# Performance work log

Hardware: AMD Instinct MI355X
Metric: run time of the kernel (lower is better)

## Reference

```python
import jax, jax.numpy as jnp
import numpy as np

B, T, C = 64, 256, 384
H = 6
D = C // H  # head_size = 64


def setup_inputs() -> dict:
    key = jax.random.key(0)
    ks = jax.random.split(key, 6)
    s = 1.0 / np.sqrt(C)
    return {
        "x": jax.random.normal(ks[0], (B, T, C), dtype=jnp.float32),
        "Wk": jax.random.uniform(ks[1], (C, C), jnp.float32, -s, s),
        "Wq": jax.random.uniform(ks[2], (C, C), jnp.float32, -s, s),
        "Wv": jax.random.uniform(ks[3], (C, C), jnp.float32, -s, s),
        "Wo": jax.random.uniform(ks[4], (C, C), jnp.float32, -s, s),
        "bo": jax.random.uniform(ks[5], (C,), jnp.float32, -s, s),
    }


def reference(x, Wk, Wq, Wv, Wo, bo):
    b, t, c = x.shape
    # QKV projections (no bias), split heads: [B, H, T, D]
    k = (x @ Wk.T).reshape(b, t, H, D).transpose(0, 2, 1, 3)
    q = (x @ Wq.T).reshape(b, t, H, D).transpose(0, 2, 1, 3)
    v = (x @ Wv.T).reshape(b, t, H, D).transpose(0, 2, 1, 3)
    # Scores scaled by C**-0.5 (as in the original module, not head_size**-0.5)
    wei = jnp.einsum("bhqd,bhkd->bhqk", q, k) * (c ** -0.5)
    mask = jnp.tril(jnp.ones((t, t), dtype=bool))
    wei = jnp.where(mask, wei, -jnp.inf)
    wei = jax.nn.softmax(wei, axis=-1)
    out = jnp.einsum("bhqk,bhkd->bhqd", wei, v)
    out = out.transpose(0, 2, 1, 3).reshape(b, t, c)
    # Output projection (dropout is identity at inference)
    return out @ Wo.T + bo
```

## Files before the change

### kernel.cpp

```cpp
#include <hip/hip_runtime.h>
#include <hip/hip_bf16.h>

typedef unsigned short u16;
typedef __attribute__((ext_vector_type(8))) short short8;
typedef __attribute__((ext_vector_type(4))) float f32x4;

#define BATCH 64
#define SEQ   256
#define CDIM  384
#define NHEAD 6
#define DHEAD 64
#define NROW  16384

constexpr float SCALE = 0.051031036307982884f;

__device__ __forceinline__ f32x4 mfma16(short8 a, short8 b, f32x4 c) {
    return __builtin_amdgcn_mfma_f32_16x16x32_bf16(a, b, c, 0, 0, 0);
}

__device__ __forceinline__ u16 f2b(float f) {
    __hip_bfloat16 h = __float2bfloat16(f);
    return *reinterpret_cast<u16*>(&h);
}

__device__ __forceinline__ void gload_lds16(const u16* g, u16* l) {
    __builtin_amdgcn_global_load_lds(
        (const __attribute__((address_space(1))) void*)g,
        (__attribute__((address_space(3))) void*)l, 16, 0, 0);
}

__global__ __launch_bounds__(256) void cvt_x(
        const float* __restrict__ s, u16* __restrict__ d)
{
    const int i = (blockIdx.x * 256 + threadIdx.x) * 8;
    const float4 a = *(const float4*)(s + i);
    const float4 b = *(const float4*)(s + i + 4);
    short8 r;
    r[0] = (short)f2b(a.x); r[1] = (short)f2b(a.y);
    r[2] = (short)f2b(a.z); r[3] = (short)f2b(a.w);
    r[4] = (short)f2b(b.x); r[5] = (short)f2b(b.y);
    r[6] = (short)f2b(b.z); r[7] = (short)f2b(b.w);
    *(short8*)(d + i) = r;
}

__global__ __launch_bounds__(256) void cvt_w(
        const float* __restrict__ w0, const float* __restrict__ w1,
        const float* __restrict__ w2, const float* __restrict__ w3,
        u16* __restrict__ d0, u16* __restrict__ d1,
        u16* __restrict__ d2, u16* __restrict__ d3)
{
    const int z = blockIdx.y;
    const float* s = (z == 0) ? w0 : (z == 1) ? w1 : (z == 2) ? w2 : w3;
    u16*         d = (z == 0) ? d0 : (z == 1) ? d1 : (z == 2) ? d2 : d3;
    const int i = (blockIdx.x * 256 + threadIdx.x) * 8;
    const float4 a = *(const float4*)(s + i);
    const float4 b = *(const float4*)(s + i + 4);
    short8 r;
    r[0] = (short)f2b(a.x); r[1] = (short)f2b(a.y);
    r[2] = (short)f2b(a.z); r[3] = (short)f2b(a.w);
    r[4] = (short)f2b(b.x); r[5] = (short)f2b(b.y);
    r[6] = (short)f2b(b.z); r[7] = (short)f2b(b.w);
    *(short8*)(d + i) = r;
}

__global__ __launch_bounds__(256) void gemm_qkv(
        const u16* __restrict__ X, const u16* __restrict__ Wk,
        const u16* __restrict__ Wv, const u16* __restrict__ Wq,
        u16* __restrict__ Kd, u16* __restrict__ VTd, u16* __restrict__ Qd)
{
    __shared__ u16 SMEM[17408];
    u16* As = SMEM;
    u16* Bs = SMEM + 4096;

    const int n0 = blockIdx.x * 128;
    const int m0 = blockIdx.y * 128;
    const int z  = blockIdx.z;
    const u16* W = (z == 0) ? Wk : (z == 1 ? Wv : Wq);

    const int tid  = threadIdx.x;
    const int lane = tid & 63;
    const int wv   = tid >> 6;
    const int l15  = lane & 15;
    const int q4   = lane >> 4;
    const int wm   = (wv >> 1) * 64;
    const int wn   = (wv & 1) * 64;

    f32x4 acc[4][4] = {};

    for (int kk = 0; kk < CDIM; kk += 32) {
        __syncthreads();
#pragma unroll
        for (int ch = 0; ch < 2; ++ch) {
            const int f = (ch * 256 + tid) * 8;
            const int r = f >> 5;
            const int c = f & 31;
            const int lb = (ch * 256 + wv * 64) * 8;
            gload_lds16(X + (size_t)(m0 + r) * CDIM + kk + c, As + lb);
            gload_lds16(W + (size_t)(n0 + r) * CDIM + kk + c, Bs + lb);
        }
        __syncthreads();

        short8 af[4], bf[4];
#pragma unroll
        for (int t = 0; t < 4; ++t) {
            af[t] = *(const short8*)(As + (wm + t * 16 + l15) * 32 + q4 * 8);
            bf[t] = *(const short8*)(Bs + (wn + t * 16 + l15) * 32 + q4 * 8);
        }
#pragma unroll
        for (int tm = 0; tm < 4; ++tm)
#pragma unroll
            for (int tn = 0; tn < 4; ++tn)
                acc[tm][tn] = mfma16(af[tm], bf[tn], acc[tm][tn]);
    }

    if (z != 1) {
        u16* D = (z == 0) ? Kd : Qd;
#pragma unroll
        for (int tm = 0; tm < 4; ++tm)
#pragma unroll
            for (int tn = 0; tn < 4; ++tn) {
                const int col = n0 + wn + tn * 16 + l15;
#pragma unroll
                for (int r = 0; r < 4; ++r) {
                    const int row = m0 + wm + tm * 16 + q4 * 4 + r;
                    const int b = row >> 8, t = row & 255;
                    const int h = col >> 6, d = col & 63;
                    D[(size_t)((b * NHEAD + h) * SEQ + t) * DHEAD + d] =
                        f2b(acc[tm][tn][r]);
                }
            }
    } else {
        __syncthreads();
        u16* T = SMEM;
#pragma unroll
        for (int tm = 0; tm < 4; ++tm)
#pragma unroll
            for (int tn = 0; tn < 4; ++tn) {
                const int cl = wn + tn * 16 + l15;
#pragma unroll
                for (int r = 0; r < 4; ++r) {
                    const int rl = wm + tm * 16 + q4 * 4 + r;
                    T[cl * 136 + rl] = f2b(acc[tm][tn][r]);
                }
            }
        __syncthreads();
        const int b  = m0 >> 8;
        const int t0 = m0 & 255;
        const int fl = tid >> 1;
        const int hf = tid & 1;
        const int fg = n0 + fl;
        const int h  = fg >> 6, d = fg & 63;
        u16* dst = VTd + ((size_t)(b * NHEAD + h) * DHEAD + d) * SEQ + t0 + hf * 64;
        const u16* src = T + fl * 136 + hf * 64;
#pragma unroll
        for (int j = 0; j < 8; ++j)
            *(uint4*)(dst + j * 8) = *(const uint4*)(src + j * 8);
    }
}

template <int CH>
__device__ __forceinline__ void attn_body(
        const u16* __restrict__ Qg, const u16* __restrict__ Kg,
        const u16* __restrict__ VTg, u16* __restrict__ Og, int bh,
        u16* SA, u16* Pbuf)
{
    constexpr int NKEY = 64 * (CH + 1);
    constexpr int KT   = NKEY / 16;
    constexpr int NPH  = (NKEY + 127) / 128;

    const int tid  = threadIdx.x;
    const int wv   = tid >> 6;
    const int lane = tid & 63;
    const int l15  = lane & 15;
    const int q4   = lane >> 4;
    const int qrow0 = CH * 64 + wv * 16;
    const int qmax  = qrow0 + 15;

    short8 aq[2];
#pragma unroll
    for (int ks = 0; ks < 2; ++ks)
        aq[ks] = *(const short8*)(Qg + (size_t)(bh * SEQ + qrow0 + l15) * DHEAD
                                     + ks * 32 + q4 * 8);

    u16* Kbuf = SA;
    f32x4 s[KT];
#pragma unroll
    for (int ph = 0; ph < NPH; ++ph) {
        const int rows = (NKEY - ph * 128) < 128 ? (NKEY - ph * 128) : 128;
        for (int it = 0; it < rows / 32; ++it) {
            const int r  = it * 32 + (tid >> 3);
            const int d0 = (tid & 7) * 8;
            *(uint4*)(Kbuf + r * 72 + d0) =
                *(const uint4*)(Kg + (size_t)(bh * SEQ + ph * 128 + r) * DHEAD + d0);
        }
        __syncthreads();
#pragma unroll
        for (int t = 0; t < rows / 16; ++t) {
            const int gt = ph * 8 + t;
            if (gt * 16 <= qmax) {
                f32x4 z = {0.f, 0.f, 0.f, 0.f};
#pragma unroll
                for (int ks = 0; ks < 2; ++ks) {
                    short8 bk = *(const short8*)(Kbuf + (t * 16 + l15) * 72
                                                 + ks * 32 + q4 * 8);
                    z = mfma16(aq[ks], bk, z);
                }
                const int kc = gt * 16 + l15;
#pragma unroll
                for (int r = 0; r < 4; ++r) {
                    float v = z[r] * SCALE;
                    if (kc > qrow0 + q4 * 4 + r) v = -1e30f;
                    z[r] = v;
                }
                s[gt] = z;
            } else {
                f32x4 neg = {-1e30f, -1e30f, -1e30f, -1e30f};
                s[gt] = neg;
            }
        }
        __syncthreads();
    }

    float mx[4], sm[4], rs[4];
#pragma unroll
    for (int r = 0; r < 4; ++r) {
        float m = -1e30f;
#pragma unroll
        for (int t = 0; t < KT; ++t) m = fmaxf(m, s[t][r]);
#pragma unroll
        for (int off = 1; off < 16; off <<= 1)
            m = fmaxf(m, __shfl_xor(m, off, 16));
        mx[r] = m;
        sm[r] = 0.f;
    }
#pragma unroll
    for (int t = 0; t < KT; ++t)
#pragma unroll
        for (int r = 0; r < 4; ++r) {
            float p = __expf(s[t][r] - mx[r]);
            s[t][r] = p;
            sm[r] += p;
        }
#pragma unroll
    for (int r = 0; r < 4; ++r) {
#pragma unroll
        for (int off = 1; off < 16; off <<= 1)
            sm[r] += __shfl_xor(sm[r], off, 16);
        rs[r] = 1.f / sm[r];
    }

    u16* Vt = SA;
    u16* Pw = Pbuf + wv * 16 * 40;
    f32x4 o[4] = {};
#pragma unroll
    for (int ph = 0; ph < NPH; ++ph) {
        const int rows = (NKEY - ph * 128) < 128 ? (NKEY - ph * 128) : 128;
        const int cpr  = rows >> 3;
#pragma unroll
        for (int it = 0; it < 4; ++it) {
            if (it < cpr / 4) {
                const int flat = it * 256 + tid;
                const int rd = flat / cpr;
                const int kc = (flat - rd * cpr) * 8;
                *(uint4*)(Vt + rd * 136 + kc) =
                    *(const uint4*)(VTg + ((size_t)bh * DHEAD + rd) * SEQ
                                        + ph * 128 + kc);
            }
        }
        __syncthreads();
#pragma unroll
        for (int ks = 0; ks < rows / 32; ++ks) {
            const int gks = ph * 4 + ks;
            if (gks * 32 <= qmax) {
#pragma unroll
                for (int tt = 0; tt < 2; ++tt) {
                    const int gt = gks * 2 + tt;
#pragma unroll
                    for (int r = 0; r < 4; ++r)
                        Pw[(q4 * 4 + r) * 40 + tt * 16 + l15] = f2b(s[gt][r]);
                }
                asm volatile("s_waitcnt lgkmcnt(0)" ::: "memory");
                short8 ap = *(const short8*)(Pw + l15 * 40 + q4 * 8);
#pragma unroll
                for (int tn = 0; tn < 4; ++tn) {
                    short8 bv = *(const short8*)(Vt + (tn * 16 + l15) * 136
                                                 + ks * 32 + q4 * 8);
                    o[tn] = mfma16(ap, bv, o[tn]);
                }
            }
        }
        __syncthreads();
    }

#pragma unroll
    for (int tn = 0; tn < 4; ++tn) {
        const int d = tn * 16 + l15;
#pragma unroll
        for (int r = 0; r < 4; ++r) {
            const int qr = qrow0 + q4 * 4 + r;
            Og[(size_t)(bh * SEQ + qr) * DHEAD + d] = f2b(o[tn][r] * rs[r]);
        }
    }
}

__global__ __launch_bounds__(256) void attn_kernel(
        const u16* __restrict__ Qg, const u16* __restrict__ Kg,
        const u16* __restrict__ VTg, u16* __restrict__ Og)
{
    __shared__ u16 SA[128 * 72];
    __shared__ u16 Pbuf[4 * 16 * 40];
    const int bh = blockIdx.y;
    switch (blockIdx.x) {
        case 0: attn_body<0>(Qg, Kg, VTg, Og, bh, SA, Pbuf); break;
        case 1: attn_body<1>(Qg, Kg, VTg, Og, bh, SA, Pbuf); break;
        case 2: attn_body<2>(Qg, Kg, VTg, Og, bh, SA, Pbuf); break;
        default: attn_body<3>(Qg, Kg, VTg, Og, bh, SA, Pbuf); break;
    }
}

__global__ __launch_bounds__(256) void gemm_out(
        const u16* __restrict__ O, const u16* __restrict__ Wo,
        const float* __restrict__ bias, float* __restrict__ out)
{
    __shared__ u16 As[128 * 32];
    __shared__ u16 Bs[128 * 32];

    const int n0 = blockIdx.x * 128;
    const int m0 = blockIdx.y * 128;

    const int tid  = threadIdx.x;
    const int lane = tid & 63;
    const int wv   = tid >> 6;
    const int l15  = lane & 15;
    const int q4   = lane >> 4;
    const int wm   = (wv >> 1) * 64;
    const int wn   = (wv & 1) * 64;

    f32x4 acc[4][4] = {};

    for (int kk = 0; kk < CDIM; kk += 32) {
        __syncthreads();
#pragma unroll
        for (int ch = 0; ch < 2; ++ch) {
            const int f = (ch * 256 + tid) * 8;
            const int r = f >> 5;
            const int c = f & 31;
            const int row = m0 + r;
            const int b = row >> 8, t = row & 255;
            const int k = kk + c;
            const int hh = k >> 6, dd = k & 63;
            const int lb = (ch * 256 + wv * 64) * 8;
            gload_lds16(O + (size_t)((b * NHEAD + hh) * SEQ + t) * DHEAD + dd,
                        As + lb);
            gload_lds16(Wo + (size_t)(n0 + r) * CDIM + kk + c, Bs + lb);
        }
        __syncthreads();

        short8 af[4], bf[4];
#pragma unroll
        for (int t = 0; t < 4; ++t) {
            af[t] = *(const short8*)(As + (wm + t * 16 + l15) * 32 + q4 * 8);
            bf[t] = *(const short8*)(Bs + (wn + t * 16 + l15) * 32 + q4 * 8);
        }
#pragma unroll
        for (int tm = 0; tm < 4; ++tm)
#pragma unroll
            for (int tn = 0; tn < 4; ++tn)
                acc[tm][tn] = mfma16(af[tm], bf[tn], acc[tm][tn]);
    }

#pragma unroll
    for (int tm = 0; tm < 4; ++tm) {
#pragma unroll
        for (int tn = 0; tn < 4; ++tn) {
            const int col = n0 + wn + tn * 16 + l15;
            const float bb = bias[col];
#pragma unroll
            for (int r = 0; r < 4; ++r) {
                const int row = m0 + wm + tm * 16 + q4 * 4 + r;
                out[(size_t)row * CDIM + col] = acc[tm][tn][r] + bb;
            }
        }
    }
}

extern "C" void kernel_launch(void* const* d_in, const int* in_sizes, int n_in,
                              void* d_out, int out_size, void* d_ws, size_t ws_size,
                              hipStream_t stream)
{
    const float* x  = (const float*)d_in[0];
    const float* Wk = (const float*)d_in[1];
    const float* Wq = (const float*)d_in[2];
    const float* Wv = (const float*)d_in[3];
    const float* Wo = (const float*)d_in[4];
    const float* bo = (const float*)d_in[5];
    float* out = (float*)d_out;

    const size_t SZ = (size_t)NROW * CDIM;
    const size_t WZ = (size_t)CDIM * CDIM;
    u16* xb  = (u16*)d_ws;
    u16* Wkb = xb  + SZ;
    u16* Wqb = Wkb + WZ;
    u16* Wvb = Wqb + WZ;
    u16* Wob = Wvb + WZ;
    u16* Kw  = Wob + WZ;
    u16* Qw  = Kw + SZ;
    u16* Ow  = Qw + SZ;
    u16* VTw = (u16*)d_out;

    cvt_x<<<dim3((int)(SZ / 2048)), 256, 0, stream>>>(x, xb);
    cvt_w<<<dim3((int)(WZ / 2048), 4), 256, 0, stream>>>(
        Wk, Wq, Wv, Wo, Wkb, Wqb, Wvb, Wob);

    dim3 g1(CDIM / 128, NROW / 128, 3);
    gemm_qkv<<<g1, 256, 0, stream>>>(xb, Wkb, Wvb, Wqb, Kw, VTw, Qw);

    dim3 g2(4, BATCH * NHEAD);
    attn_kernel<<<g2, 256, 0, stream>>>(Qw, Kw, VTw, Ow);

    dim3 g3(CDIM / 128, NROW / 128);
    gemm_out<<<g3, 256, 0, stream>>>(Ow, Wob, bo, out);
}
```

Measured before the change: 158.2 us.

## Merge conversion kernels, deepen GEMM K-tiles to 64 with XOR-swizzled LDS

```diff
diff --git a/kernel.cpp b/kernel.cpp
--- a/kernel.cpp
+++ b/kernel.cpp
@@ -29,10 +29,27 @@
         (__attribute__((address_space(3))) void*)l, 16, 0, 0);
 }
 
-__global__ __launch_bounds__(256) void cvt_x(
-        const float* __restrict__ s, u16* __restrict__ d)
-{
-    const int i = (blockIdx.x * 256 + threadIdx.x) * 8;
+__global__ __launch_bounds__(256) void cvt_all(
+        const float* __restrict__ x,
+        const float* __restrict__ Wk, const float* __restrict__ Wq,
+        const float* __restrict__ Wv, const float* __restrict__ Wo,
+        u16* __restrict__ xb,
+        u16* __restrict__ wkb, u16* __restrict__ wqb,
+        u16* __restrict__ wvb, u16* __restrict__ wob)
+{
+    int blk = blockIdx.x;
+    const float* s;
+    u16* d;
+    if (blk < 3072) {
+        s = x; d = xb;
+    } else {
+        const int w = blk - 3072;
+        const int z = w / 72;
+        blk = w - z * 72;
+        s = (z == 0) ? Wk : (z == 1) ? Wq : (z == 2) ? Wv : Wo;
+        d = (z == 0) ? wkb : (z == 1) ? wqb : (z == 2) ? wvb : wob;
+    }
+    const int i = (blk * 256 + threadIdx.x) * 8;
     const float4 a = *(const float4*)(s + i);
     const float4 b = *(const float4*)(s + i + 4);
     short8 r;
@@ -43,26 +60,6 @@
     *(short8*)(d + i) = r;
 }
 
-__global__ __launch_bounds__(256) void cvt_w(
-        const float* __restrict__ w0, const float* __restrict__ w1,
-        const float* __restrict__ w2, const float* __restrict__ w3,
-        u16* __restrict__ d0, u16* __restrict__ d1,
-        u16* __restrict__ d2, u16* __restrict__ d3)
-{
-    const int z = blockIdx.y;
-    const float* s = (z == 0) ? w0 : (z == 1) ? w1 : (z == 2) ? w2 : w3;
-    u16*         d = (z == 0) ? d0 : (z == 1) ? d1 : (z == 2) ? d2 : d3;
-    const int i = (blockIdx.x * 256 + threadIdx.x) * 8;
-    const float4 a = *(const float4*)(s + i);
-    const float4 b = *(const float4*)(s + i + 4);
-    short8 r;
-    r[0] = (short)f2b(a.x); r[1] = (short)f2b(a.y);
-    r[2] = (short)f2b(a.z); r[3] = (short)f2b(a.w);
-    r[4] = (short)f2b(b.x); r[5] = (short)f2b(b.y);
-    r[6] = (short)f2b(b.z); r[7] = (short)f2b(b.w);
-    *(short8*)(d + i) = r;
-}
-
 __global__ __launch_bounds__(256) void gemm_qkv(
         const u16* __restrict__ X, const u16* __restrict__ Wk,
         const u16* __restrict__ Wv, const u16* __restrict__ Wq,
@@ -70,7 +67,7 @@
 {
     __shared__ u16 SMEM[17408];
     u16* As = SMEM;
-    u16* Bs = SMEM + 4096;
+    u16* Bs = SMEM + 8192;
 
     const int n0 = blockIdx.x * 128;
     const int m0 = blockIdx.y * 128;
@@ -87,30 +84,37 @@
 
     f32x4 acc[4][4] = {};
 
-    for (int kk = 0; kk < CDIM; kk += 32) {
-        __syncthreads();
-#pragma unroll
-        for (int ch = 0; ch < 2; ++ch) {
+    for (int kk = 0; kk < CDIM; kk += 64) {
+        __syncthreads();
+#pragma unroll
+        for (int ch = 0; ch < 4; ++ch) {
             const int f = (ch * 256 + tid) * 8;
-            const int r = f >> 5;
-            const int c = f & 31;
+            const int r = f >> 6;
+            const int c = (f ^ ((r & 7) << 3)) & 63;
             const int lb = (ch * 256 + wv * 64) * 8;
             gload_lds16(X + (size_t)(m0 + r) * CDIM + kk + c, As + lb);
             gload_lds16(W + (size_t)(n0 + r) * CDIM + kk + c, Bs + lb);
         }
         __syncthreads();
 
-        short8 af[4], bf[4];
-#pragma unroll
-        for (int t = 0; t < 4; ++t) {
-            af[t] = *(const short8*)(As + (wm + t * 16 + l15) * 32 + q4 * 8);
-            bf[t] = *(const short8*)(Bs + (wn + t * 16 + l15) * 32 + q4 * 8);
-        }
-#pragma unroll
-        for (int tm = 0; tm < 4; ++tm)
-#pragma unroll
-            for (int tn = 0; tn < 4; ++tn)
-                acc[tm][tn] = mfma16(af[tm], bf[tn], acc[tm][tn]);
+#pragma unroll
+        for (int ks = 0; ks < 2; ++ks) {
+            short8 af[4], bf[4];
+#pragma unroll
+            for (int t = 0; t < 4; ++t) {
+                const int ra = wm + t * 16 + l15;
+                const int rb = wn + t * 16 + l15;
+                af[t] = *(const short8*)(As + ra * 64 +
+                        ((ks * 32 + q4 * 8) ^ ((ra & 7) << 3)));
+                bf[t] = *(const short8*)(Bs + rb * 64 +
+                        ((ks * 32 + q4 * 8) ^ ((rb & 7) << 3)));
+            }
+#pragma unroll
+            for (int tm = 0; tm < 4; ++tm)
+#pragma unroll
+                for (int tn = 0; tn < 4; ++tn)
+                    acc[tm][tn] = mfma16(af[tm], bf[tn], acc[tm][tn]);
+        }
     }
 
     if (z != 1) {
@@ -322,55 +326,67 @@
         const u16* __restrict__ O, const u16* __restrict__ Wo,
         const float* __restrict__ bias, float* __restrict__ out)
 {
-    __shared__ u16 As[128 * 32];
-    __shared__ u16 Bs[128 * 32];
+    __shared__ u16 As[64 * 64];
+    __shared__ u16 Bs[128 * 64];
 
     const int n0 = blockIdx.x * 128;
-    const int m0 = blockIdx.y * 128;
+    const int m0 = blockIdx.y * 64;
 
     const int tid  = threadIdx.x;
     const int lane = tid & 63;
     const int wv   = tid >> 6;
     const int l15  = lane & 15;
     const int q4   = lane >> 4;
-    const int wm   = (wv >> 1) * 64;
+    const int wm   = (wv >> 1) * 32;
     const int wn   = (wv & 1) * 64;
 
-    f32x4 acc[4][4] = {};
-
-    for (int kk = 0; kk < CDIM; kk += 32) {
-        __syncthreads();
-#pragma unroll
-        for (int ch = 0; ch < 2; ++ch) {
+    f32x4 acc[2][4] = {};
+
+    for (int kk = 0; kk < CDIM; kk += 64) {
+        __syncthreads();
+#pragma unroll
+        for (int ch = 0; ch < 4; ++ch) {
             const int f = (ch * 256 + tid) * 8;
-            const int r = f >> 5;
-            const int c = f & 31;
-            const int row = m0 + r;
-            const int b = row >> 8, t = row & 255;
-            const int k = kk + c;
-            const int hh = k >> 6, dd = k & 63;
+            const int r = f >> 6;
+            const int c = (f ^ ((r & 7) << 3)) & 63;
             const int lb = (ch * 256 + wv * 64) * 8;
-            gload_lds16(O + (size_t)((b * NHEAD + hh) * SEQ + t) * DHEAD + dd,
-                        As + lb);
             gload_lds16(Wo + (size_t)(n0 + r) * CDIM + kk + c, Bs + lb);
-        }
-        __syncthreads();
-
-        short8 af[4], bf[4];
-#pragma unroll
-        for (int t = 0; t < 4; ++t) {
-            af[t] = *(const short8*)(As + (wm + t * 16 + l15) * 32 + q4 * 8);
-            bf[t] = *(const short8*)(Bs + (wn + t * 16 + l15) * 32 + q4 * 8);
-        }
-#pragma unroll
-        for (int tm = 0; tm < 4; ++tm)
-#pragma unroll
-            for (int tn = 0; tn < 4; ++tn)
-                acc[tm][tn] = mfma16(af[tm], bf[tn], acc[tm][tn]);
-    }
-
-#pragma unroll
-    for (int tm = 0; tm < 4; ++tm) {
+            if (ch < 2) {
+                const int row = m0 + r;
+                const int b = row >> 8, t = row & 255;
+                const int k = kk + c;
+                const int hh = k >> 6, dd = k & 63;
+                gload_lds16(O + (size_t)((b * NHEAD + hh) * SEQ + t) * DHEAD + dd,
+                            As + lb);
+            }
+        }
+        __syncthreads();
+
+#pragma unroll
+        for (int ks = 0; ks < 2; ++ks) {
+            short8 af[2], bf[4];
+#pragma unroll
+            for (int t = 0; t < 2; ++t) {
+                const int ra = wm + t * 16 + l15;
+                af[t] = *(const short8*)(As + ra * 64 +
+                        ((ks * 32 + q4 * 8) ^ ((ra & 7) << 3)));
+            }
+#pragma unroll
+            for (int t = 0; t < 4; ++t) {
+                const int rb = wn + t * 16 + l15;
+                bf[t] = *(const short8*)(Bs + rb * 64 +
+                        ((ks * 32 + q4 * 8) ^ ((rb & 7) << 3)));
+            }
+#pragma unroll
+            for (int tm = 0; tm < 2; ++tm)
+#pragma unroll
+                for (int tn = 0; tn < 4; ++tn)
+                    acc[tm][tn] = mfma16(af[tm], bf[tn], acc[tm][tn]);
+        }
+    }
+
+#pragma unroll
+    for (int tm = 0; tm < 2; ++tm) {
 #pragma unroll
         for (int tn = 0; tn < 4; ++tn) {
             const int col = n0 + wn + tn * 16 + l15;
@@ -408,9 +424,8 @@
     u16* Ow  = Qw + SZ;
     u16* VTw = (u16*)d_out;
 
-    cvt_x<<<dim3((int)(SZ / 2048)), 256, 0, stream>>>(x, xb);
-    cvt_w<<<dim3((int)(WZ / 2048), 4), 256, 0, stream>>>(
-        Wk, Wq, Wv, Wo, Wkb, Wqb, Wvb, Wob);
+    cvt_all<<<dim3(3360), 256, 0, stream>>>(
+        x, Wk, Wq, Wv, Wo, xb, Wkb, Wqb, Wvb, Wob);
 
     dim3 g1(CDIM / 128, NROW / 128, 3);
     gemm_qkv<<<g1, 256, 0, stream>>>(xb, Wkb, Wvb, Wqb, Kw, VTw, Qw);
@@ -418,6 +433,6 @@
     dim3 g2(4, BATCH * NHEAD);
     attn_kernel<<<g2, 256, 0, stream>>>(Qw, Kw, VTw, Ow);
 
-    dim3 g3(CDIM / 128, NROW / 128);
+    dim3 g3(CDIM / 128, NROW / 64);
     gemm_out<<<g3, 256, 0, stream>>>(Ow, Wob, bo, out);
 }
```

Result: no change. 156.0 us (-1.3%).
